# Kernel tuning notes

Hardware: AMD Instinct MI355X
Metric: run time of the kernel (lower is better)

## Reference

```python
import jax, jax.numpy as jnp
import numpy as np

CHUNK = 128      # chunk_size
NUM_BITS = 6     # log2(num_experts=64)


def setup_inputs() -> dict:
    key = jax.random.key(0)
    k1, k2, k3 = jax.random.split(key, 3)
    B, L, D, E = 4, 4096, 1024, 64
    x = jax.random.normal(k1, (B, L, D), dtype=jnp.float32)
    expert_weights = jax.random.normal(k2, (E, D, D), dtype=jnp.float32) * 0.02
    hyperplanes = jax.random.normal(k3, (D, NUM_BITS), dtype=jnp.float32)
    return {"x": x, "expert_weights": expert_weights, "hyperplanes": hyperplanes}


def reference(x, expert_weights, hyperplanes):
    # x: [B, L, D]; L divisible by CHUNK (no padding path taken)
    B, L, D = x.shape
    C = L // CHUNK
    xr = x.reshape(B, C, CHUNK, D)

    # --- LSH (SimHash) router, chunk-level ---
    chunk_emb = xr.mean(axis=2)                      # [B, C, D]
    proj = chunk_emb @ hyperplanes                   # [B, C, bits]
    bits = (proj > 0).astype(jnp.int32)
    powers = (2 ** jnp.arange(NUM_BITS)).astype(jnp.int32)
    e1 = jnp.sum(bits * powers, axis=-1)             # [B, C]
    weakest = jnp.argmin(jnp.abs(proj), axis=-1)     # weakest hyperplane bit
    flip = (2 ** weakest).astype(jnp.int32)
    e2 = jnp.bitwise_xor(e1, flip)                   # second expert: flip weakest bit
    # gates are all 1.0 and router_threshold=0.0 -> confidence_mask = 1.0

    # --- per-chunk expert weight gather + bmm combine (top-2 average) ---
    out = jnp.zeros_like(xr)
    for idx in (e1, e2):
        w = expert_weights[idx]                      # [B, C, D, D] gathered
        out = out + jnp.einsum('bcld,bcde->bcle', xr, w)
    out = out * 0.5
    # dropout p=0.0 / eval -> identity
    return out.reshape(B, L, D)
```

## Files before the change

kernel.cpp:

```cpp
#include <hip/hip_runtime.h>
#include <hip/hip_bf16.h>


#define BD 4
#define LD 4096
#define DD 1024
#define ED 64
#define CHUNKD 128
#define NBITS 6
#define NCHUNK 128

typedef __bf16 bf16_8 __attribute__((ext_vector_type(8)));
typedef __bf16 bf16_4 __attribute__((ext_vector_type(4)));
typedef float floatx4 __attribute__((ext_vector_type(4)));

#define WT_PER_ENT  131072

__global__ __launch_bounds__(256) void sum_cvt_kernel(
    const float* __restrict__ x, __bf16* __restrict__ a, double* __restrict__ csum_p)
{
    const int chunk = blockIdx.x >> 3;
    const int tg = blockIdx.x & 7;
    const size_t base = (size_t)chunk * CHUNKD * DD + (size_t)tg * 16 * DD;
    const float* xc = x + base;
    __bf16* ac = a + base;
    const int t = threadIdx.x;

    double s0 = 0, s1 = 0, s2 = 0, s3 = 0;
    #pragma unroll 4
    for (int tok = 0; tok < 16; ++tok) {
        const float4 v = *(const float4*)(xc + tok * DD + t * 4);
        bf16_4 o;
        o[0] = (__bf16)v.x; o[1] = (__bf16)v.y; o[2] = (__bf16)v.z; o[3] = (__bf16)v.w;
        *(bf16_4*)(ac + tok * DD + t * 4) = o;
        s0 += (double)v.x; s1 += (double)v.y; s2 += (double)v.z; s3 += (double)v.w;
    }
    double* c = csum_p + ((size_t)(chunk * 8 + tg)) * DD + t * 4;
    c[0] = s0; c[1] = s1; c[2] = s2; c[3] = s3;
}

__global__ __launch_bounds__(256) void router2_kernel(
    const double* __restrict__ csum_p, const float* __restrict__ hyp,
    int* __restrict__ eidx)
{
    const int chunk = blockIdx.x;
    const int t = threadIdx.x;
    double pj[NBITS];
    #pragma unroll
    for (int j = 0; j < NBITS; ++j) pj[j] = 0.0;
    #pragma unroll
    for (int i = 0; i < 4; ++i) {
        const int d = t + i * 256;
        double cs = 0.0;
        #pragma unroll
        for (int tg = 0; tg < 8; ++tg)
            cs += csum_p[((size_t)(chunk * 8 + tg)) * DD + d];
        const double emb = cs * (1.0 / 128.0);
        #pragma unroll
        for (int j = 0; j < NBITS; ++j)
            pj[j] += emb * (double)hyp[d * NBITS + j];
    }
    #pragma unroll
    for (int off = 32; off > 0; off >>= 1) {
        #pragma unroll
        for (int j = 0; j < NBITS; ++j)
            pj[j] += __shfl_down(pj[j], off, 64);
    }
    __shared__ double red[4][NBITS];
    const int wave = t >> 6, lane = t & 63;
    if (lane == 0) {
        #pragma unroll
        for (int j = 0; j < NBITS; ++j) red[wave][j] = pj[j];
    }
    __syncthreads();
    if (t == 0) {
        int e1 = 0, weakest = 0;
        double best = 1e300;
        #pragma unroll
        for (int j = 0; j < NBITS; ++j) {
            double p = red[0][j] + red[1][j] + red[2][j] + red[3][j];
            if (p > 0.0) e1 |= (1 << j);
            double aa = fabs(p);
            if (aa < best) { best = aa; weakest = j; }
        }
        eidx[chunk * 2 + 0] = e1;
        eidx[chunk * 2 + 1] = e1 ^ (1 << weakest);
    }
}

__global__ __launch_bounds__(256) void wcvt_kernel(
    const float* __restrict__ W, __bf16* __restrict__ WtSw,
    const int* __restrict__ eidx)
{
    __shared__ float tile[32 * 129];
    __shared__ int s_used;

    const int bx = blockIdx.x;
    const int kh = bx & 1;
    const int nt = (bx >> 1) & 7;
    const int e  = bx >> 4;
    const int t = threadIdx.x;

    if (t == 0) s_used = 0;
    __syncthreads();
    if (eidx[t] == e) s_used = 1;
    __syncthreads();
    if (!s_used) return;

    const float* We = W + (size_t)e * DD * DD + nt * 128;
    __bf16* base_ent = WtSw + (size_t)(e * 8 + nt) * WT_PER_ENT;

    for (int it = 0; it < 16; ++it) {
        const int k0 = kh * 512 + it * 32;
        const int s  = kh * 16 + it;
        #pragma unroll
        for (int p = 0; p < 4; ++p) {
            const int idx = p * 256 + t;
            const int kr  = idx >> 5;
            const int nc4 = idx & 31;
            const float4 v = *(const float4*)(We + (size_t)(k0 + kr) * DD + nc4 * 4);
            float* dst = &tile[kr * 129 + nc4 * 4];
            dst[0] = v.x; dst[1] = v.y; dst[2] = v.z; dst[3] = v.w;
        }
        __syncthreads();
        #pragma unroll
        for (int c = 0; c < 2; ++c) {
            const int cell = c * 256 + t;
            const int l  = cell & 63;
            const int rb = cell >> 6;
            const int q  = l >> 4;
            const int lr = l & 15;
            bf16_8 o;
            #pragma unroll
            for (int j = 0; j < 8; ++j)
                o[j] = (__bf16)tile[(q * 8 + j) * 129 + rb * 16 + lr];
            *(bf16_8*)(base_ent + ((size_t)s * 8 + rb) * 512 + l * 8) = o;
        }
        __syncthreads();
    }
}

__global__ __launch_bounds__(256) void ffn_gemm_bf16(
    const __bf16* __restrict__ Abf,
    const __bf16* __restrict__ WtSw,
    const int* __restrict__ eidx,
    float* __restrict__ out)
{
    __shared__ __bf16 Als[8 * 512];
    __shared__ __bf16 B0ls[8 * 512];
    __shared__ __bf16 B1ls[8 * 512];

    const int bx = blockIdx.x;
    const int chunk = bx >> 3;
    const int ntb = bx & 7;
    const int t = threadIdx.x;
    const int lane = t & 63;
    const int wave = t >> 6;
    const int wm = wave >> 1;
    const int wn = wave & 1;
    const int lr = lane & 15;
    const int q  = lane >> 4;

    const int e0 = eidx[chunk * 2 + 0];
    const int e1 = eidx[chunk * 2 + 1];

    const __bf16* Ag = Abf + (size_t)chunk * CHUNKD * DD;
    const __bf16* Bg0 = WtSw + (size_t)(e0 * 8 + ntb) * WT_PER_ENT + lane * 8;
    const __bf16* Bg1 = WtSw + (size_t)(e1 * 8 + ntb) * WT_PER_ENT + lane * 8;

    const int rb0 = wave * 2;
    const __bf16* AgW0 = Ag + (size_t)(rb0 * 16 + lr) * DD + q * 8;
    const __bf16* AgW1 = Ag + (size_t)((rb0 + 1) * 16 + lr) * DD + q * 8;

    floatx4 acc[4][4] = {};

    for (int ks = 0; ks < 32; ++ks) {
        const int k0 = ks * 32;
        __builtin_amdgcn_global_load_lds(
            (const __attribute__((address_space(1))) void*)(AgW0 + k0),
            (__attribute__((address_space(3))) void*)(&Als[rb0 * 512]), 16, 0, 0);
        __builtin_amdgcn_global_load_lds(
            (const __attribute__((address_space(1))) void*)(AgW1 + k0),
            (__attribute__((address_space(3))) void*)(&Als[(rb0 + 1) * 512]), 16, 0, 0);
        #pragma unroll
        for (int i = 0; i < 2; ++i) {
            const int rb = rb0 + i;
            __builtin_amdgcn_global_load_lds(
                (const __attribute__((address_space(1))) void*)(Bg0 + ((size_t)ks * 8 + rb) * 512),
                (__attribute__((address_space(3))) void*)(&B0ls[rb * 512]), 16, 0, 0);
            __builtin_amdgcn_global_load_lds(
                (const __attribute__((address_space(1))) void*)(Bg1 + ((size_t)ks * 8 + rb) * 512),
                (__attribute__((address_space(3))) void*)(&B1ls[rb * 512]), 16, 0, 0);
        }
        __syncthreads();

        bf16_8 af[4], bb[4];
        #pragma unroll
        for (int mt = 0; mt < 4; ++mt)
            af[mt] = *(const bf16_8*)(&Als[(wm * 4 + mt) * 512 + lane * 8]);
        #pragma unroll
        for (int nt = 0; nt < 4; ++nt)
            bb[nt] = *(const bf16_8*)(&B0ls[(wn * 4 + nt) * 512 + lane * 8]);
        #pragma unroll
        for (int mt = 0; mt < 4; ++mt) {
            #pragma unroll
            for (int nt = 0; nt < 4; ++nt)
                acc[mt][nt] = __builtin_amdgcn_mfma_f32_16x16x32_bf16(
                    af[mt], bb[nt], acc[mt][nt], 0, 0, 0);
        }
        #pragma unroll
        for (int nt = 0; nt < 4; ++nt)
            bb[nt] = *(const bf16_8*)(&B1ls[(wn * 4 + nt) * 512 + lane * 8]);
        #pragma unroll
        for (int mt = 0; mt < 4; ++mt) {
            #pragma unroll
            for (int nt = 0; nt < 4; ++nt)
                acc[mt][nt] = __builtin_amdgcn_mfma_f32_16x16x32_bf16(
                    af[mt], bb[nt], acc[mt][nt], 0, 0, 0);
        }
        __syncthreads();
    }

    const size_t orow0 = (size_t)chunk * CHUNKD;
    const int n0 = ntb * 128;
    #pragma unroll
    for (int mt = 0; mt < 4; ++mt) {
        #pragma unroll
        for (int nt = 0; nt < 4; ++nt) {
            const int col = n0 + wn * 64 + nt * 16 + lr;
            #pragma unroll
            for (int r = 0; r < 4; ++r) {
                const int row = wm * 64 + mt * 16 + q * 4 + r;
                out[(orow0 + row) * DD + col] = acc[mt][nt][r] * 0.5f;
            }
        }
    }
}

__global__ __launch_bounds__(256) void router_kernel(
    const float* __restrict__ x, const float* __restrict__ hyp,
    int* __restrict__ eidx)
{
    const int chunk = blockIdx.x;
    const int t = threadIdx.x;
    const float* xc = x + (size_t)chunk * CHUNKD * DD;
    double cs[4] = {0.0, 0.0, 0.0, 0.0};
    for (int tok = 0; tok < CHUNKD; ++tok) {
        const float* row = xc + tok * DD;
        #pragma unroll
        for (int i = 0; i < 4; ++i) cs[i] += (double)row[t + i * 256];
    }
    double pj[NBITS];
    #pragma unroll
    for (int j = 0; j < NBITS; ++j) pj[j] = 0.0;
    #pragma unroll
    for (int i = 0; i < 4; ++i) {
        const int d = t + i * 256;
        const double emb = cs[i] * (1.0 / 128.0);
        #pragma unroll
        for (int j = 0; j < NBITS; ++j) pj[j] += emb * (double)hyp[d * NBITS + j];
    }
    #pragma unroll
    for (int off = 32; off > 0; off >>= 1) {
        #pragma unroll
        for (int j = 0; j < NBITS; ++j) pj[j] += __shfl_down(pj[j], off, 64);
    }
    __shared__ double red[4][NBITS];
    const int wave = t >> 6, lane = t & 63;
    if (lane == 0) {
        #pragma unroll
        for (int j = 0; j < NBITS; ++j) red[wave][j] = pj[j];
    }
    __syncthreads();
    if (t == 0) {
        int e1 = 0, weakest = 0;
        double best = 1e300;
        #pragma unroll
        for (int j = 0; j < NBITS; ++j) {
            double p = red[0][j] + red[1][j] + red[2][j] + red[3][j];
            if (p > 0.0) e1 |= (1 << j);
            double a = fabs(p);
            if (a < best) { best = a; weakest = j; }
        }
        eidx[chunk * 2 + 0] = e1;
        eidx[chunk * 2 + 1] = e1 ^ (1 << weakest);
    }
}

__global__ __launch_bounds__(256) void cvt_x_kernel(
    const float* __restrict__ x, __bf16* __restrict__ a)
{
    const size_t i = ((size_t)blockIdx.x * 256 + threadIdx.x) * 4;
    const float4 v = *(const float4*)(x + i);
    bf16_4 o;
    o[0] = (__bf16)v.x; o[1] = (__bf16)v.y; o[2] = (__bf16)v.z; o[3] = (__bf16)v.w;
    *(bf16_4*)(a + i) = o;
}

__global__ __launch_bounds__(256) void ffn_gemm_fp32w(
    const __bf16* __restrict__ Abf, const float* __restrict__ W,
    const int* __restrict__ eidx, float* __restrict__ out)
{
    __shared__ __bf16 Als[128 * 32];
    __shared__ __bf16 Bls[128 * 32];
    const int bx = blockIdx.x;
    const int chunk = bx >> 3;
    const int n0 = (bx & 7) * 128;
    const int t = threadIdx.x;
    const int lane = t & 63;
    const int wave = t >> 6;
    const int wm = wave >> 1;
    const int wn = wave & 1;
    const int lr = lane & 15;
    const int q  = lane >> 4;
    const int ee[2] = {eidx[chunk * 2 + 0], eidx[chunk * 2 + 1]};
    const __bf16* Ag = Abf + (size_t)chunk * CHUNKD * DD;
    const int a_col = (lane & 3) * 8;
    const int a_rsub = lane >> 2;
    floatx4 acc[4][4] = {};
    for (int xp = 0; xp < 2; ++xp) {
        const float* We = W + (size_t)ee[xp] * (DD * DD) + n0;
        for (int k0 = 0; k0 < DD; k0 += 32) {
            float bv[2][8];
            #pragma unroll
            for (int rep = 0; rep < 2; ++rep) {
                const int nb = wave * 16 + lr + rep * 64;
                const float* src = We + (size_t)(k0 + q * 8) * DD + nb;
                #pragma unroll
                for (int j = 0; j < 8; ++j) bv[rep][j] = src[(size_t)j * DD];
            }
            #pragma unroll
            for (int i = 0; i < 2; ++i) {
                const __bf16* ga = Ag + (size_t)((wave * 2 + i) * 16 + a_rsub) * DD + k0 + a_col;
                __builtin_amdgcn_global_load_lds(
                    (const __attribute__((address_space(1))) void*)ga,
                    (__attribute__((address_space(3))) void*)(&Als[(wave * 2 + i) * 512]),
                    16, 0, 0);
            }
            #pragma unroll
            for (int rep = 0; rep < 2; ++rep) {
                const int nb = wave * 16 + lr + rep * 64;
                bf16_8 bw;
                #pragma unroll
                for (int j = 0; j < 8; ++j) bw[j] = (__bf16)bv[rep][j];
                *(bf16_8*)(&Bls[nb * 32 + q * 8]) = bw;
            }
            __syncthreads();
            bf16_8 af[4], bfr[4];
            #pragma unroll
            for (int mt = 0; mt < 4; ++mt)
                af[mt] = *(const bf16_8*)(&Als[(wm * 64 + mt * 16 + lr) * 32 + q * 8]);
            #pragma unroll
            for (int nt = 0; nt < 4; ++nt)
                bfr[nt] = *(const bf16_8*)(&Bls[(wn * 64 + nt * 16 + lr) * 32 + q * 8]);
            #pragma unroll
            for (int mt = 0; mt < 4; ++mt) {
                #pragma unroll
                for (int nt = 0; nt < 4; ++nt)
                    acc[mt][nt] = __builtin_amdgcn_mfma_f32_16x16x32_bf16(
                        af[mt], bfr[nt], acc[mt][nt], 0, 0, 0);
            }
            __syncthreads();
        }
    }
    const size_t orow0 = (size_t)chunk * CHUNKD;
    #pragma unroll
    for (int mt = 0; mt < 4; ++mt) {
        #pragma unroll
        for (int nt = 0; nt < 4; ++nt) {
            const int col = n0 + wn * 64 + nt * 16 + lr;
            #pragma unroll
            for (int r = 0; r < 4; ++r) {
                const int row = wm * 64 + mt * 16 + q * 4 + r;
                out[(orow0 + row) * DD + col] = acc[mt][nt][r] * 0.5f;
            }
        }
    }
}

extern "C" void kernel_launch(void* const* d_in, const int* in_sizes, int n_in,
                              void* d_out, int out_size, void* d_ws, size_t ws_size,
                              hipStream_t stream) {
    const float* x   = (const float*)d_in[0];
    const float* W   = (const float*)d_in[1];
    const float* hyp = (const float*)d_in[2];
    float* out = (float*)d_out;

    const size_t off_eidx = 0;
    const size_t off_csum = 4096;
    const size_t off_a    = off_csum + (size_t)NCHUNK * 8 * DD * 8;
    const size_t off_wt   = off_a + (size_t)NCHUNK * CHUNKD * DD * 2;
    const size_t need     = off_wt + (size_t)ED * DD * DD * 2;

    int* eidx = (int*)((char*)d_ws + off_eidx);
    __bf16* Abf = (__bf16*)((char*)d_ws + off_a);

    if (ws_size >= need) {
        double* csum_p = (double*)((char*)d_ws + off_csum);
        __bf16* WtSw = (__bf16*)((char*)d_ws + off_wt);
        sum_cvt_kernel<<<NCHUNK * 8, 256, 0, stream>>>(x, Abf, csum_p);
        router2_kernel<<<NCHUNK, 256, 0, stream>>>(csum_p, hyp, eidx);
        wcvt_kernel<<<ED * 16, 256, 0, stream>>>(W, WtSw, eidx);
        ffn_gemm_bf16<<<NCHUNK * 8, 256, 0, stream>>>(Abf, WtSw, eidx, out);
    } else {
        __bf16* Abf2 = (__bf16*)((char*)d_ws + 1024);
        router_kernel<<<NCHUNK, 256, 0, stream>>>(x, hyp, eidx);
        cvt_x_kernel<<<(BD * LD * DD) / (256 * 4), 256, 0, stream>>>(x, Abf2);
        ffn_gemm_fp32w<<<NCHUNK * 8, 256, 0, stream>>>(Abf2, W, eidx, out);
    }
}
```

Baseline: 531.0 us.

## Double-buffer LDS tiles in expert GEMM and remap blocks per XCD

Splits the LDS tiles of the expert GEMM into two buffers, so the async global-to-LDS loads for the next K step are issued before computing on the current buffer. Partial vmcnt waits plus raw barriers replace the full __syncthreads pairs, aiming to hide global load latency behind the MFMA work. Block indices are also remapped so that all 8 column tiles of a chunk run on the same XCD, which should improve L2 reuse of the A rows. The cost is double the LDS use, which may lower occupancy, and hand-written waitcnt logic that depends on every thread issuing exactly six loads per stage.

```diff
diff --git a/kernel.cpp b/kernel.cpp
--- a/kernel.cpp
+++ b/kernel.cpp
@@ -146,13 +146,16 @@
     const int* __restrict__ eidx,
     float* __restrict__ out)
 {
-    __shared__ __bf16 Als[8 * 512];
-    __shared__ __bf16 B0ls[8 * 512];
-    __shared__ __bf16 B1ls[8 * 512];
-
-    const int bx = blockIdx.x;
-    const int chunk = bx >> 3;
-    const int ntb = bx & 7;
+    __shared__ __bf16 Als[2][8 * 512];
+    __shared__ __bf16 B0ls[2][8 * 512];
+    __shared__ __bf16 B1ls[2][8 * 512];
+
+    const int bx0 = blockIdx.x;
+    const int xcd = bx0 & 7;
+    const int jj  = bx0 >> 3;
+    const int chunk = xcd * 16 + (jj >> 3);
+    const int ntb   = jj & 7;
+
     const int t = threadIdx.x;
     const int lane = t & 63;
     const int wave = t >> 6;
@@ -174,52 +177,95 @@
 
     floatx4 acc[4][4] = {};
 
-    for (int ks = 0; ks < 32; ++ks) {
-        const int k0 = ks * 32;
-        __builtin_amdgcn_global_load_lds(
-            (const __attribute__((address_space(1))) void*)(AgW0 + k0),
-            (__attribute__((address_space(3))) void*)(&Als[rb0 * 512]), 16, 0, 0);
-        __builtin_amdgcn_global_load_lds(
-            (const __attribute__((address_space(1))) void*)(AgW1 + k0),
-            (__attribute__((address_space(3))) void*)(&Als[(rb0 + 1) * 512]), 16, 0, 0);
-        #pragma unroll
-        for (int i = 0; i < 2; ++i) {
-            const int rb = rb0 + i;
-            __builtin_amdgcn_global_load_lds(
-                (const __attribute__((address_space(1))) void*)(Bg0 + ((size_t)ks * 8 + rb) * 512),
-                (__attribute__((address_space(3))) void*)(&B0ls[rb * 512]), 16, 0, 0);
-            __builtin_amdgcn_global_load_lds(
-                (const __attribute__((address_space(1))) void*)(Bg1 + ((size_t)ks * 8 + rb) * 512),
-                (__attribute__((address_space(3))) void*)(&B1ls[rb * 512]), 16, 0, 0);
-        }
-        __syncthreads();
-
-        bf16_8 af[4], bb[4];
-        #pragma unroll
-        for (int mt = 0; mt < 4; ++mt)
-            af[mt] = *(const bf16_8*)(&Als[(wm * 4 + mt) * 512 + lane * 8]);
-        #pragma unroll
-        for (int nt = 0; nt < 4; ++nt)
-            bb[nt] = *(const bf16_8*)(&B0ls[(wn * 4 + nt) * 512 + lane * 8]);
-        #pragma unroll
-        for (int mt = 0; mt < 4; ++mt) {
-            #pragma unroll
-            for (int nt = 0; nt < 4; ++nt)
-                acc[mt][nt] = __builtin_amdgcn_mfma_f32_16x16x32_bf16(
-                    af[mt], bb[nt], acc[mt][nt], 0, 0, 0);
-        }
-        #pragma unroll
-        for (int nt = 0; nt < 4; ++nt)
-            bb[nt] = *(const bf16_8*)(&B1ls[(wn * 4 + nt) * 512 + lane * 8]);
-        #pragma unroll
-        for (int mt = 0; mt < 4; ++mt) {
-            #pragma unroll
-            for (int nt = 0; nt < 4; ++nt)
-                acc[mt][nt] = __builtin_amdgcn_mfma_f32_16x16x32_bf16(
-                    af[mt], bb[nt], acc[mt][nt], 0, 0, 0);
-        }
-        __syncthreads();
-    }
+#define STAGE(BSEL, KS) do {                                                   \
+    const int k0_ = (KS) * 32;                                                 \
+    __builtin_amdgcn_global_load_lds(                                          \
+        (const __attribute__((address_space(1))) void*)(AgW0 + k0_),           \
+        (__attribute__((address_space(3))) void*)(&Als[BSEL][rb0 * 512]), 16, 0, 0); \
+    __builtin_amdgcn_global_load_lds(                                          \
+        (const __attribute__((address_space(1))) void*)(AgW1 + k0_),           \
+        (__attribute__((address_space(3))) void*)(&Als[BSEL][(rb0 + 1) * 512]), 16, 0, 0); \
+    __builtin_amdgcn_global_load_lds(                                          \
+        (const __attribute__((address_space(1))) void*)(Bg0 + ((size_t)(KS) * 8 + rb0) * 512), \
+        (__attribute__((address_space(3))) void*)(&B0ls[BSEL][rb0 * 512]), 16, 0, 0); \
+    __builtin_amdgcn_global_load_lds(                                          \
+        (const __attribute__((address_space(1))) void*)(Bg1 + ((size_t)(KS) * 8 + rb0) * 512), \
+        (__attribute__((address_space(3))) void*)(&B1ls[BSEL][rb0 * 512]), 16, 0, 0); \
+    __builtin_amdgcn_global_load_lds(                                          \
+        (const __attribute__((address_space(1))) void*)(Bg0 + ((size_t)(KS) * 8 + rb0 + 1) * 512), \
+        (__attribute__((address_space(3))) void*)(&B0ls[BSEL][(rb0 + 1) * 512]), 16, 0, 0); \
+    __builtin_amdgcn_global_load_lds(                                          \
+        (const __attribute__((address_space(1))) void*)(Bg1 + ((size_t)(KS) * 8 + rb0 + 1) * 512), \
+        (__attribute__((address_space(3))) void*)(&B1ls[BSEL][(rb0 + 1) * 512]), 16, 0, 0); \
+} while (0)
+
+#define COMPUTE(BSEL) do {                                                     \
+    bf16_8 af[4], bb[4];                                                       \
+    _Pragma("unroll")                                                          \
+    for (int mt = 0; mt < 4; ++mt)                                             \
+        af[mt] = *(const bf16_8*)(&Als[BSEL][(wm * 4 + mt) * 512 + lane * 8]); \
+    _Pragma("unroll")                                                          \
+    for (int nt = 0; nt < 4; ++nt)                                             \
+        bb[nt] = *(const bf16_8*)(&B0ls[BSEL][(wn * 4 + nt) * 512 + lane * 8]); \
+    _Pragma("unroll")                                                          \
+    for (int mt = 0; mt < 4; ++mt) {                                           \
+        _Pragma("unroll")                                                      \
+        for (int nt = 0; nt < 4; ++nt)                                         \
+            acc[mt][nt] = __builtin_amdgcn_mfma_f32_16x16x32_bf16(             \
+                af[mt], bb[nt], acc[mt][nt], 0, 0, 0);                         \
+    }                                                                          \
+    _Pragma("unroll")                                                          \
+    for (int nt = 0; nt < 4; ++nt)                                             \
+        bb[nt] = *(const bf16_8*)(&B1ls[BSEL][(wn * 4 + nt) * 512 + lane * 8]); \
+    _Pragma("unroll")                                                          \
+    for (int mt = 0; mt < 4; ++mt) {                                           \
+        _Pragma("unroll")                                                      \
+        for (int nt = 0; nt < 4; ++nt)                                         \
+            acc[mt][nt] = __builtin_amdgcn_mfma_f32_16x16x32_bf16(             \
+                af[mt], bb[nt], acc[mt][nt], 0, 0, 0);                         \
+    }                                                                          \
+} while (0)
+
+#define BAR_ENTER_6() do {                                                     \
+    asm volatile("s_waitcnt vmcnt(6)" ::: "memory");                           \
+    __builtin_amdgcn_s_barrier();                                              \
+    asm volatile("" ::: "memory");                                             \
+} while (0)
+#define BAR_ENTER_0() do {                                                     \
+    asm volatile("s_waitcnt vmcnt(0)" ::: "memory");                           \
+    __builtin_amdgcn_s_barrier();                                              \
+    asm volatile("" ::: "memory");                                             \
+} while (0)
+#define BAR_EXIT() do {                                                        \
+    asm volatile("" ::: "memory");                                             \
+    __builtin_amdgcn_s_barrier();                                              \
+    asm volatile("" ::: "memory");                                             \
+} while (0)
+
+    STAGE(0, 0);
+    #pragma unroll 1
+    for (int ks = 0; ks < 30; ks += 2) {
+        STAGE(1, ks + 1);
+        BAR_ENTER_6();
+        COMPUTE(0);
+        BAR_EXIT();
+        STAGE(0, ks + 2);
+        BAR_ENTER_6();
+        COMPUTE(1);
+        BAR_EXIT();
+    }
+    STAGE(1, 31);
+    BAR_ENTER_6();
+    COMPUTE(0);
+    BAR_EXIT();
+    BAR_ENTER_0();
+    COMPUTE(1);
+
+#undef STAGE
+#undef COMPUTE
+#undef BAR_ENTER_6
+#undef BAR_ENTER_0
+#undef BAR_EXIT
 
     const size_t orow0 = (size_t)chunk * CHUNKD;
     const int n0 = ntb * 128;
```

New measurement: 528.6 us. About the same (-0.5%).

## Double-buffer bf16 expert GEMM with 512-thread blocks and XCD-aware chunk mapping

Applied to the files above, without the earlier changes.

Rewrites the main bf16 GEMM kernel to use 512-thread blocks computing 128x256 output tiles. It double-buffers A and B tiles in 96KB of dynamic LDS, using staged vmcnt waits and barriers so the next k-slice loads while the current MFMAs run. It also remaps block indices so each XCD handles a contiguous range of chunks for better L2 reuse, and raises MFMA wave priority. The cost is higher LDS usage per block, which lowers occupancy, plus hand-tuned waitcnt counts that are fragile.

```diff
diff --git a/kernel.cpp b/kernel.cpp
--- a/kernel.cpp
+++ b/kernel.cpp
@@ -140,89 +140,144 @@
     }
 }
 
-__global__ __launch_bounds__(256) void ffn_gemm_bf16(
+__global__ __launch_bounds__(512) void ffn_gemm_bf16(
     const __bf16* __restrict__ Abf,
     const __bf16* __restrict__ WtSw,
     const int* __restrict__ eidx,
     float* __restrict__ out)
 {
-    __shared__ __bf16 Als[8 * 512];
-    __shared__ __bf16 B0ls[8 * 512];
-    __shared__ __bf16 B1ls[8 * 512];
-
-    const int bx = blockIdx.x;
-    const int chunk = bx >> 3;
-    const int ntb = bx & 7;
+    extern __shared__ char smem[];
+    __bf16* Ab = (__bf16*)smem;
+    __bf16* Bb = (__bf16*)(smem + 32768);
+#define A_OFF(c, h, rb)      ((((c) * 2 + (h)) * 8 + (rb)) * 512)
+#define B_OFF(c, s, ntl, cb) (((((c) * 2 + (s)) * 2 + (ntl)) * 8 + (cb)) * 512)
+
+    const int bx0 = blockIdx.x;
+    const int xcd = bx0 & 7;
+    const int j = bx0 >> 3;
+    const int chunk = xcd * 16 + (j >> 2);
+    const int nb = j & 3;
+
     const int t = threadIdx.x;
     const int lane = t & 63;
     const int wave = t >> 6;
-    const int wm = wave >> 1;
-    const int wn = wave & 1;
+    const int wm = wave >> 2;
+    const int wn = wave & 3;
     const int lr = lane & 15;
     const int q  = lane >> 4;
+    const int ntl_r = wn >> 1;
+    const int cbb   = (wn & 1) * 4;
 
     const int e0 = eidx[chunk * 2 + 0];
     const int e1 = eidx[chunk * 2 + 1];
 
-    const __bf16* Ag = Abf + (size_t)chunk * CHUNKD * DD;
-    const __bf16* Bg0 = WtSw + (size_t)(e0 * 8 + ntb) * WT_PER_ENT + lane * 8;
-    const __bf16* Bg1 = WtSw + (size_t)(e1 * 8 + ntb) * WT_PER_ENT + lane * 8;
-
-    const int rb0 = wave * 2;
-    const __bf16* AgW0 = Ag + (size_t)(rb0 * 16 + lr) * DD + q * 8;
-    const __bf16* AgW1 = Ag + (size_t)((rb0 + 1) * 16 + lr) * DD + q * 8;
+    const __bf16* Ag  = Abf + (size_t)chunk * CHUNKD * DD;
+    const __bf16* AgS = Ag + (size_t)(wave * 16 + lr) * DD + q * 8;
+
+    const int ntl_s = wave >> 2;
+    const int ib    = wave & 3;
+    const int cbE   = ib + ((ib >> 1) << 1);
+    const int cbL   = cbE + 2;
+    const __bf16* BgE0 = WtSw + (size_t)(e0 * 8 + nb * 2 + ntl_s) * WT_PER_ENT + lane * 8;
+    const __bf16* BgE1 = WtSw + (size_t)(e1 * 8 + nb * 2 + ntl_s) * WT_PER_ENT + lane * 8;
 
     floatx4 acc[4][4] = {};
-
-    for (int ks = 0; ks < 32; ++ks) {
-        const int k0 = ks * 32;
-        __builtin_amdgcn_global_load_lds(
-            (const __attribute__((address_space(1))) void*)(AgW0 + k0),
-            (__attribute__((address_space(3))) void*)(&Als[rb0 * 512]), 16, 0, 0);
-        __builtin_amdgcn_global_load_lds(
-            (const __attribute__((address_space(1))) void*)(AgW1 + k0),
-            (__attribute__((address_space(3))) void*)(&Als[(rb0 + 1) * 512]), 16, 0, 0);
-        #pragma unroll
-        for (int i = 0; i < 2; ++i) {
-            const int rb = rb0 + i;
-            __builtin_amdgcn_global_load_lds(
-                (const __attribute__((address_space(1))) void*)(Bg0 + ((size_t)ks * 8 + rb) * 512),
-                (__attribute__((address_space(3))) void*)(&B0ls[rb * 512]), 16, 0, 0);
-            __builtin_amdgcn_global_load_lds(
-                (const __attribute__((address_space(1))) void*)(Bg1 + ((size_t)ks * 8 + rb) * 512),
-                (__attribute__((address_space(3))) void*)(&B1ls[rb * 512]), 16, 0, 0);
-        }
-        __syncthreads();
-
-        bf16_8 af[4], bb[4];
-        #pragma unroll
-        for (int mt = 0; mt < 4; ++mt)
-            af[mt] = *(const bf16_8*)(&Als[(wm * 4 + mt) * 512 + lane * 8]);
-        #pragma unroll
-        for (int nt = 0; nt < 4; ++nt)
-            bb[nt] = *(const bf16_8*)(&B0ls[(wn * 4 + nt) * 512 + lane * 8]);
-        #pragma unroll
-        for (int mt = 0; mt < 4; ++mt) {
-            #pragma unroll
-            for (int nt = 0; nt < 4; ++nt)
-                acc[mt][nt] = __builtin_amdgcn_mfma_f32_16x16x32_bf16(
-                    af[mt], bb[nt], acc[mt][nt], 0, 0, 0);
-        }
-        #pragma unroll
-        for (int nt = 0; nt < 4; ++nt)
-            bb[nt] = *(const bf16_8*)(&B1ls[(wn * 4 + nt) * 512 + lane * 8]);
-        #pragma unroll
-        for (int mt = 0; mt < 4; ++mt) {
-            #pragma unroll
-            for (int nt = 0; nt < 4; ++nt)
-                acc[mt][nt] = __builtin_amdgcn_mfma_f32_16x16x32_bf16(
-                    af[mt], bb[nt], acc[mt][nt], 0, 0, 0);
-        }
-        __syncthreads();
-    }
+    bf16_8 af[4], bbv[2];
+
+#define ISSUE_A(c, tt, h)                                                      \
+    __builtin_amdgcn_global_load_lds(                                          \
+        (const __attribute__((address_space(1))) void*)(AgS + ((tt) & 15) * 64 + (h) * 32), \
+        (__attribute__((address_space(3))) void*)(&Ab[A_OFF(c, h, wave)]), 16, 0, 0)
+
+#define ISSUE_B(c, tt, s, cb) do {                                             \
+    const __bf16* bsrc_ = ((tt) < 16 ? BgE0 : BgE1)                            \
+        + ((size_t)((((tt) & 15) * 2 + (s)) * 8 + (cb))) * 512;                \
+    __builtin_amdgcn_global_load_lds(                                          \
+        (const __attribute__((address_space(1))) void*)bsrc_,                  \
+        (__attribute__((address_space(3))) void*)(&Bb[B_OFF(c, s, ntl_s, cb)]), 16, 0, 0); \
+} while (0)
+
+#define DS_AF(c, h) do {                                                       \
+    _Pragma("unroll")                                                          \
+    for (int mt = 0; mt < 4; ++mt)                                             \
+        af[mt] = *(const bf16_8*)(&Ab[A_OFF(c, h, wm * 4 + mt) + lane * 8]);   \
+} while (0)
+
+#define DS_BB(c, s, ntA, ntB) do {                                             \
+    bbv[0] = *(const bf16_8*)(&Bb[B_OFF(c, s, ntl_r, cbb + (ntA)) + lane * 8]); \
+    bbv[1] = *(const bf16_8*)(&Bb[B_OFF(c, s, ntl_r, cbb + (ntB)) + lane * 8]); \
+} while (0)
+
+#define MFMA8(ntA, ntB) do {                                                   \
+    __builtin_amdgcn_s_setprio(1);                                             \
+    _Pragma("unroll")                                                          \
+    for (int mt = 0; mt < 4; ++mt) {                                           \
+        acc[mt][ntA] = __builtin_amdgcn_mfma_f32_16x16x32_bf16(                \
+            af[mt], bbv[0], acc[mt][ntA], 0, 0, 0);                            \
+        acc[mt][ntB] = __builtin_amdgcn_mfma_f32_16x16x32_bf16(                \
+            af[mt], bbv[1], acc[mt][ntB], 0, 0, 0);                            \
+    }                                                                          \
+    __builtin_amdgcn_s_setprio(0);                                             \
+} while (0)
+
+#define VBAR(N) do {                                                           \
+    asm volatile("s_waitcnt vmcnt(" #N ")" ::: "memory");                      \
+    __builtin_amdgcn_s_barrier();                                              \
+} while (0)
+
+    ISSUE_A(0, 0, 0);
+    ISSUE_B(0, 0, 0, cbE);
+    ISSUE_B(0, 0, 0, cbL);
+    ISSUE_A(0, 0, 1);
+    ISSUE_B(0, 0, 1, cbE);
+    ISSUE_B(0, 0, 1, cbL);
+    VBAR(4);
+
+    #pragma unroll 1
+    for (int tt = 0; tt < 31; ++tt) {
+        const int c  = tt & 1;
+        const int nx = c ^ 1;
+        DS_AF(c, 0); DS_BB(c, 0, 0, 1);
+        ISSUE_A(nx, tt + 1, 0); ISSUE_B(nx, tt + 1, 0, cbE);
+        VBAR(5);
+        MFMA8(0, 1);
+        DS_BB(c, 0, 2, 3);
+        ISSUE_B(nx, tt + 1, 0, cbL); ISSUE_A(nx, tt + 1, 1);
+        VBAR(5);
+        MFMA8(2, 3);
+        DS_AF(c, 1); DS_BB(c, 1, 0, 1);
+        ISSUE_B(nx, tt + 1, 1, cbE); ISSUE_B(nx, tt + 1, 1, cbL);
+        VBAR(6);
+        MFMA8(0, 1);
+        DS_BB(c, 1, 2, 3);
+        VBAR(4);
+        MFMA8(2, 3);
+    }
+    {
+        DS_AF(1, 0); DS_BB(1, 0, 0, 1);
+        VBAR(3);
+        MFMA8(0, 1);
+        DS_BB(1, 0, 2, 3);
+        VBAR(1);
+        MFMA8(2, 3);
+        DS_AF(1, 1); DS_BB(1, 1, 0, 1);
+        VBAR(0);
+        MFMA8(0, 1);
+        DS_BB(1, 1, 2, 3);
+        MFMA8(2, 3);
+    }
+
+#undef ISSUE_A
+#undef ISSUE_B
+#undef DS_AF
+#undef DS_BB
+#undef MFMA8
+#undef VBAR
+#undef A_OFF
+#undef B_OFF
 
     const size_t orow0 = (size_t)chunk * CHUNKD;
-    const int n0 = ntb * 128;
+    const int n0 = nb * 256;
     #pragma unroll
     for (int mt = 0; mt < 4; ++mt) {
         #pragma unroll
@@ -346,10 +401,10 @@
                 *(bf16_8*)(&Bls[nb * 32 + q * 8]) = bw;
             }
             __syncthreads();
-            bf16_8 af[4], bfr[4];
+            bf16_8 af2[4], bfr[4];
             #pragma unroll
             for (int mt = 0; mt < 4; ++mt)
-                af[mt] = *(const bf16_8*)(&Als[(wm * 64 + mt * 16 + lr) * 32 + q * 8]);
+                af2[mt] = *(const bf16_8*)(&Als[(wm * 64 + mt * 16 + lr) * 32 + q * 8]);
             #pragma unroll
             for (int nt = 0; nt < 4; ++nt)
                 bfr[nt] = *(const bf16_8*)(&Bls[(wn * 64 + nt * 16 + lr) * 32 + q * 8]);
@@ -358,7 +413,7 @@
                 #pragma unroll
                 for (int nt = 0; nt < 4; ++nt)
                     acc[mt][nt] = __builtin_amdgcn_mfma_f32_16x16x32_bf16(
-                        af[mt], bfr[nt], acc[mt][nt], 0, 0, 0);
+                        af2[mt], bfr[nt], acc[mt][nt], 0, 0, 0);
             }
             __syncthreads();
         }
@@ -401,7 +456,7 @@
         sum_cvt_kernel<<<NCHUNK * 8, 256, 0, stream>>>(x, Abf, csum_p);
         router2_kernel<<<NCHUNK, 256, 0, stream>>>(csum_p, hyp, eidx);
         wcvt_kernel<<<ED * 16, 256, 0, stream>>>(W, WtSw, eidx);
-        ffn_gemm_bf16<<<NCHUNK * 8, 256, 0, stream>>>(Abf, WtSw, eidx, out);
+        ffn_gemm_bf16<<<512, 512, 98304, stream>>>(Abf, WtSw, eidx, out);
     } else {
         __bf16* Abf2 = (__bf16*)((char*)d_ws + 1024);
         router_kernel<<<NCHUNK, 256, 0, stream>>>(x, hyp, eidx);
```

After: 529.7 us. No clear change (-0.2%).

## Sort chunks by primary expert and map them to XCDs for L2 weight reuse

Applied to the files above, without the earlier changes.

Block 0 of the weight-conversion kernel runs a serial counting sort that orders chunks by their primary expert and writes the resulting permutation. The GEMM kernel then maps each block to a chunk through this permutation, so each XCD (chosen by blockIdx mod 8) handles 16 consecutive sorted chunks. Chunks that share an expert therefore land on the same XCD's L2 and can reuse the converted expert weights. The cost is a single-threaded sort of 128 entries added to one block's critical path, plus an extra indirection when each GEMM block starts.

```diff
diff --git a/kernel.cpp b/kernel.cpp
--- a/kernel.cpp
+++ b/kernel.cpp
@@ -90,16 +90,27 @@
 
 __global__ __launch_bounds__(256) void wcvt_kernel(
     const float* __restrict__ W, __bf16* __restrict__ WtSw,
-    const int* __restrict__ eidx)
+    const int* __restrict__ eidx, int* __restrict__ perm)
 {
     __shared__ float tile[32 * 129];
     __shared__ int s_used;
+    __shared__ int sortbuf[128];
 
     const int bx = blockIdx.x;
     const int kh = bx & 1;
     const int nt = (bx >> 1) & 7;
     const int e  = bx >> 4;
     const int t = threadIdx.x;
+
+    if (bx == 0 && t == 0) {
+        int* cnt = sortbuf;
+        int* pos = sortbuf + 64;
+        for (int i = 0; i < 64; ++i) cnt[i] = 0;
+        for (int c = 0; c < NCHUNK; ++c) cnt[eidx[c * 2]]++;
+        int s = 0;
+        for (int i = 0; i < 64; ++i) { pos[i] = s; s += cnt[i]; }
+        for (int c = 0; c < NCHUNK; ++c) perm[pos[eidx[c * 2]]++] = c;
+    }
 
     if (t == 0) s_used = 0;
     __syncthreads();
@@ -144,6 +155,7 @@
     const __bf16* __restrict__ Abf,
     const __bf16* __restrict__ WtSw,
     const int* __restrict__ eidx,
+    const int* __restrict__ perm,
     float* __restrict__ out)
 {
     __shared__ __bf16 Als[8 * 512];
@@ -151,8 +163,11 @@
     __shared__ __bf16 B1ls[8 * 512];
 
     const int bx = blockIdx.x;
-    const int chunk = bx >> 3;
-    const int ntb = bx & 7;
+    const int xcd = bx & 7;
+    const int g = bx >> 3;
+    const int chunk = perm[xcd * 16 + (g >> 3)];
+    const int ntb = g & 7;
+
     const int t = threadIdx.x;
     const int lane = t & 63;
     const int wave = t >> 6;
@@ -346,10 +361,10 @@
                 *(bf16_8*)(&Bls[nb * 32 + q * 8]) = bw;
             }
             __syncthreads();
-            bf16_8 af[4], bfr[4];
+            bf16_8 af2[4], bfr[4];
             #pragma unroll
             for (int mt = 0; mt < 4; ++mt)
-                af[mt] = *(const bf16_8*)(&Als[(wm * 64 + mt * 16 + lr) * 32 + q * 8]);
+                af2[mt] = *(const bf16_8*)(&Als[(wm * 64 + mt * 16 + lr) * 32 + q * 8]);
             #pragma unroll
             for (int nt = 0; nt < 4; ++nt)
                 bfr[nt] = *(const bf16_8*)(&Bls[(wn * 64 + nt * 16 + lr) * 32 + q * 8]);
@@ -358,7 +373,7 @@
                 #pragma unroll
                 for (int nt = 0; nt < 4; ++nt)
                     acc[mt][nt] = __builtin_amdgcn_mfma_f32_16x16x32_bf16(
-                        af[mt], bfr[nt], acc[mt][nt], 0, 0, 0);
+                        af2[mt], bfr[nt], acc[mt][nt], 0, 0, 0);
             }
             __syncthreads();
         }
@@ -387,12 +402,14 @@
     float* out = (float*)d_out;
 
     const size_t off_eidx = 0;
+    const size_t off_perm = 2048;
     const size_t off_csum = 4096;
     const size_t off_a    = off_csum + (size_t)NCHUNK * 8 * DD * 8;
     const size_t off_wt   = off_a + (size_t)NCHUNK * CHUNKD * DD * 2;
     const size_t need     = off_wt + (size_t)ED * DD * DD * 2;
 
     int* eidx = (int*)((char*)d_ws + off_eidx);
+    int* perm = (int*)((char*)d_ws + off_perm);
     __bf16* Abf = (__bf16*)((char*)d_ws + off_a);
 
     if (ws_size >= need) {
@@ -400,8 +417,8 @@
         __bf16* WtSw = (__bf16*)((char*)d_ws + off_wt);
         sum_cvt_kernel<<<NCHUNK * 8, 256, 0, stream>>>(x, Abf, csum_p);
         router2_kernel<<<NCHUNK, 256, 0, stream>>>(csum_p, hyp, eidx);
-        wcvt_kernel<<<ED * 16, 256, 0, stream>>>(W, WtSw, eidx);
-        ffn_gemm_bf16<<<NCHUNK * 8, 256, 0, stream>>>(Abf, WtSw, eidx, out);
+        wcvt_kernel<<<ED * 16, 256, 0, stream>>>(W, WtSw, eidx, perm);
+        ffn_gemm_bf16<<<NCHUNK * 8, 256, 0, stream>>>(Abf, WtSw, eidx, perm, out);
     } else {
         __bf16* Abf2 = (__bf16*)((char*)d_ws + 1024);
         router_kernel<<<NCHUNK, 256, 0, stream>>>(x, hyp, eidx);
```

Result: no change. 527.6 us (-0.6%).
